# Performance work log

Hardware: AMD Instinct MI355X
Metric: run time of the kernel (lower is better)

Reference implementation:

```python
import jax, jax.numpy as jnp
import numpy as np

N_NODES = 100000
N_EDGES = 1600000
D_IN = 128
D_OUT = 128


def setup_inputs() -> dict:
    key = jax.random.key(0)
    ks = jax.random.split(key, 8)
    h = jax.random.normal(ks[0], (N_NODES, D_IN), dtype=jnp.float32)
    edge_val = jax.random.uniform(ks[1], (N_EDGES,), dtype=jnp.float32)
    # Linear weights in torch layout [out, in]
    W_self = jax.random.normal(ks[2], (D_OUT, D_IN), dtype=jnp.float32) * (1.0 / np.sqrt(D_IN))
    b_self = jax.random.normal(ks[3], (D_OUT,), dtype=jnp.float32) * 0.01
    W_nb = jax.random.normal(ks[4], (D_OUT, D_IN), dtype=jnp.float32) * (1.0 / np.sqrt(D_IN))
    b_nb = jax.random.normal(ks[5], (D_OUT,), dtype=jnp.float32) * 0.01
    edge_row = jax.random.randint(ks[6], (N_EDGES,), 0, N_NODES, dtype=jnp.int64)
    edge_col = jax.random.randint(ks[7], (N_EDGES,), 0, N_NODES, dtype=jnp.int64)
    return {"h": h, "edge_val": edge_val, "W_self": W_self, "b_self": b_self,
            "W_nb": W_nb, "b_nb": b_nb, "edge_row": edge_row, "edge_col": edge_col}


def reference(h, edge_val, W_self, b_self, W_nb, b_nb, edge_row, edge_col):
    # self_h = Linear_self(h[:out_nodes]); out_nodes == N_NODES here
    self_h = h @ W_self.T + b_self  # [N, D_OUT]
    # neighbor_h = adj.spmm(h): sparse COO (row, col, val) times dense h
    msgs = edge_val[:, None] * h[edge_col]            # [E, D_IN]
    neighbor_h = jax.ops.segment_sum(msgs, edge_row, num_segments=N_NODES)  # [N, D_IN]
    out = self_h + neighbor_h @ W_nb.T + b_nb
    return out
```

## Files before the change

kernel.cpp:

```cpp
#include <hip/hip_runtime.h>


constexpr int NN = 100000;
constexpr int NE = 1600000;
constexpr int D  = 128;
constexpr int NBUCK  = 391;
constexpr int BCAP   = 4608;
constexpr int CHUNK  = 4096;
constexpr int NCH    = (NE + CHUNK - 1) / CHUNK;
constexpr int GM     = 64;
constexpr int NGB    = (NN + GM - 1) / GM;
constexpr int LP     = 132;

typedef __bf16 bf16x8 __attribute__((ext_vector_type(8)));
typedef float  f32x4  __attribute__((ext_vector_type(4)));
typedef float  f32x2  __attribute__((ext_vector_type(2)));

__global__ __launch_bounds__(256) void gemm_mfma(
    const float* __restrict__ h,
    const float* __restrict__ Wself,
    const float* __restrict__ Wnb,
    const float* __restrict__ bself,
    const float* __restrict__ bnb,
    float* __restrict__ out,
    __bf16* __restrict__ tmpb)
{
    __shared__ __bf16 hs[GM * LP];
    const int t    = threadIdx.x;
    const int w    = t >> 6;
    const int lane = t & 63;
    const int l15  = lane & 15;
    const int quad = lane >> 4;
    const int row0 = blockIdx.x * GM;

    #pragma unroll
    for (int it = 0; it < 4; ++it) {
        int idx = it * 2048 + t * 8;
        int r = idx >> 7, c = idx & 127;
        int gr = row0 + r; if (gr >= NN) gr = NN - 1;
        f32x4 lo = *(const f32x4*)(h + (size_t)gr * D + c);
        f32x4 hi = *(const f32x4*)(h + (size_t)gr * D + c + 4);
        bf16x8 v;
        #pragma unroll
        for (int j = 0; j < 4; ++j) { v[j] = (__bf16)lo[j]; v[4 + j] = (__bf16)hi[j]; }
        *(bf16x8*)(hs + r * LP + c) = v;
    }

    bf16x8 b[4][4];
    #pragma unroll
    for (int ns = 0; ns < 4; ++ns) {
        int wrow = w * 64 + ns * 16 + l15;
        const float* wr = (wrow < D) ? (Wself + (size_t)wrow * D)
                                     : (Wnb + (size_t)(wrow - D) * D);
        #pragma unroll
        for (int kk = 0; kk < 4; ++kk) {
            f32x4 lo = *(const f32x4*)(wr + kk * 32 + quad * 8);
            f32x4 hi = *(const f32x4*)(wr + kk * 32 + quad * 8 + 4);
            bf16x8 bb;
            #pragma unroll
            for (int j = 0; j < 4; ++j) { bb[j] = (__bf16)lo[j]; bb[4 + j] = (__bf16)hi[j]; }
            b[ns][kk] = bb;
        }
    }
    float bias[4];
    #pragma unroll
    for (int ns = 0; ns < 4; ++ns) {
        int col = w * 64 + ns * 16 + l15;
        bias[ns] = (col < D) ? (bself[col] + bnb[col]) : 0.f;
    }
    __syncthreads();

    f32x4 acc[4][4];
    #pragma unroll
    for (int mi = 0; mi < 4; ++mi)
        #pragma unroll
        for (int ns = 0; ns < 4; ++ns) acc[mi][ns] = (f32x4){0.f, 0.f, 0.f, 0.f};

    #pragma unroll
    for (int mi = 0; mi < 4; ++mi) {
        bf16x8 afr[4];
        #pragma unroll
        for (int kk = 0; kk < 4; ++kk)
            afr[kk] = *(const bf16x8*)(hs + (mi * 16 + l15) * LP + quad * 8 + kk * 32);
        #pragma unroll
        for (int ns = 0; ns < 4; ++ns)
            #pragma unroll
            for (int kk = 0; kk < 4; ++kk)
                acc[mi][ns] = __builtin_amdgcn_mfma_f32_16x16x32_bf16(afr[kk], b[ns][kk], acc[mi][ns], 0, 0, 0);
    }

    #pragma unroll
    for (int mi = 0; mi < 4; ++mi) {
        if (w < 2) {
            #pragma unroll
            for (int ns = 0; ns < 4; ++ns) {
                int col = w * 64 + ns * 16 + l15;
                #pragma unroll
                for (int i = 0; i < 4; ++i) {
                    int row = row0 + mi * 16 + quad * 4 + i;
                    if (row < NN) out[(size_t)row * D + col] = acc[mi][ns][i] + bias[ns];
                }
            }
        } else {
            #pragma unroll
            for (int ns = 0; ns < 4; ++ns) {
                int col = w * 64 + ns * 16 + l15 - D;
                #pragma unroll
                for (int i = 0; i < 4; ++i) {
                    int row = row0 + mi * 16 + quad * 4 + i;
                    if (row < NN) tmpb[(size_t)row * D + col] = (__bf16)acc[mi][ns][i];
                }
            }
        }
    }
}

__global__ __launch_bounds__(512) void wc_scatter(
    const int* __restrict__ erow, const int* __restrict__ ecol,
    const float* __restrict__ eval_,
    int* __restrict__ gcount, int2* __restrict__ epair)
{
    __shared__ int  cnt[NBUCK];
    __shared__ int  lscan[NBUCK];
    __shared__ int  gbase[NBUCK];
    __shared__ int  ss[512];
    __shared__ int2 sbuf[CHUNK];
    __shared__ int  saddr[CHUNK];
    __shared__ int  s_total;

    const int t  = threadIdx.x;
    const int c0 = blockIdx.x * CHUNK;

    for (int b = t; b < NBUCK; b += 512) cnt[b] = 0;
    __syncthreads();

    int   bp[8];
    int   colr[8];
    float valr[8];
    #pragma unroll
    for (int j = 0; j < 8; ++j) {
        int e = c0 + j * 512 + t;
        if (e < NE) {
            int r   = erow[e];
            colr[j] = ecol[e];
            valr[j] = eval_[e];
            int b   = r >> 8;
            int pos = atomicAdd(&cnt[b], 1);
            bp[j]   = b | ((r & 255) << 9) | (pos << 17);
        } else bp[j] = -1;
    }
    __syncthreads();

    ss[t] = (t < NBUCK) ? cnt[t] : 0;
    __syncthreads();
    for (int off = 1; off < 512; off <<= 1) {
        int y = (t >= off) ? ss[t - off] : 0;
        __syncthreads();
        ss[t] += y;
        __syncthreads();
    }
    if (t < NBUCK) {
        int n = cnt[t];
        lscan[t] = ss[t] - n;
        gbase[t] = (n > 0) ? atomicAdd(&gcount[t], n) : 0;
    }
    if (t == 0) s_total = ss[511];
    __syncthreads();

    #pragma unroll
    for (int j = 0; j < 8; ++j) {
        if (bp[j] >= 0) {
            int b   = bp[j] & 511;
            int rlo = (bp[j] >> 9) & 255;
            int pos = bp[j] >> 17;
            int slot = lscan[b] + pos;
            sbuf[slot]  = make_int2(colr[j] | (rlo << 17), __float_as_int(valr[j]));
            saddr[slot] = b * BCAP + gbase[b] + pos;
        }
    }
    __syncthreads();

    int ce = s_total;
    for (int i = t; i < ce; i += 512)
        epair[saddr[i]] = sbuf[i];
}

__global__ __launch_bounds__(512) void bucket_sort(
    const int2* __restrict__ epair, const int* __restrict__ gcount,
    int2* __restrict__ epair2, int2* __restrict__ rowrange)
{
    __shared__ int  cnt[256];
    __shared__ int  off2[256];
    __shared__ int  cur[256];
    __shared__ int  ss[256];
    __shared__ int2 sorted[BCAP];

    const int t = threadIdx.x;
    const int b = blockIdx.x;
    const int n = gcount[b];
    const int2* src = epair + (size_t)b * BCAP;

    if (t < 256) cnt[t] = 0;
    __syncthreads();

    int2 r[9];
    int  nr = 0;
    for (int i = t; i < n; i += 512) {
        int2 p = src[i];
        r[nr++] = p;
        atomicAdd(&cnt[(p.x >> 17) & 255], 1);
    }
    __syncthreads();

    if (t < 256) ss[t] = cnt[t];
    __syncthreads();
    for (int o = 1; o < 256; o <<= 1) {
        int y = 0;
        if (t < 256 && t >= o) y = ss[t - o];
        __syncthreads();
        if (t < 256) ss[t] += y;
        __syncthreads();
    }
    if (t < 256) {
        int v = cnt[t];
        off2[t] = ss[t] - v;
        cur[t]  = ss[t] - v;
    }
    __syncthreads();

    for (int j = 0; j < nr; ++j) {
        int slot = atomicAdd(&cur[(r[j].x >> 17) & 255], 1);
        sorted[slot] = r[j];
    }
    __syncthreads();

    const int base = b * BCAP;
    for (int i = t; i < n; i += 512)
        epair2[base + i] = sorted[i];
    if (t < 256) {
        int row = b * 256 + t;
        if (row < NN)
            rowrange[row] = make_int2(base + off2[t], base + off2[t] + cnt[t]);
    }
}

__global__ __launch_bounds__(256) void aggregate(
    const __bf16* __restrict__ tmpb, const int2* __restrict__ rowrange,
    const int2* __restrict__ epair2, float* __restrict__ out,
    int row0, int nrows)
{
    int wave = row0 + ((blockIdx.x * 256 + threadIdx.x) >> 6);
    if (wave >= row0 + nrows) return;
    int lane = threadIdx.x & 63;
    int2 rr = rowrange[wave];
    int beg = __builtin_amdgcn_readfirstlane(rr.x);
    int end = __builtin_amdgcn_readfirstlane(rr.y);

    float ax[4] = {0.f, 0.f, 0.f, 0.f};
    float ay[4] = {0.f, 0.f, 0.f, 0.f};
    int e = beg;
    for (; e + 3 < end; e += 4) {
        int2 p[4];
        #pragma unroll
        for (int k = 0; k < 4; ++k) p[k] = epair2[e + k];
        #pragma unroll
        for (int k = 0; k < 4; ++k) {
            int col = p[k].x & 0x1FFFF;
            unsigned u = *(const unsigned*)(tmpb + (size_t)col * D + lane * 2);
            float v = __int_as_float(p[k].y);
            ax[k] += v * __uint_as_float(u << 16);
            ay[k] += v * __uint_as_float(u & 0xffff0000u);
        }
    }
    for (; e < end; ++e) {
        int2 p = epair2[e];
        int col = p.x & 0x1FFFF;
        unsigned u = *(const unsigned*)(tmpb + (size_t)col * D + lane * 2);
        float v = __int_as_float(p.y);
        ax[0] += v * __uint_as_float(u << 16);
        ay[0] += v * __uint_as_float(u & 0xffff0000u);
    }
    f32x2* o = (f32x2*)(out + (size_t)wave * D + lane * 2);
    f32x2 c = __builtin_nontemporal_load(o);
    c.x += (ax[0] + ax[1]) + (ax[2] + ax[3]);
    c.y += (ay[0] + ay[1]) + (ay[2] + ay[3]);
    __builtin_nontemporal_store(c, o);
}

extern "C" void kernel_launch(void* const* d_in, const int* in_sizes, int n_in,
                              void* d_out, int out_size, void* d_ws, size_t ws_size,
                              hipStream_t stream) {
    const float* h     = (const float*)d_in[0];
    const float* eval_ = (const float*)d_in[1];
    const float* Wself = (const float*)d_in[2];
    const float* bself = (const float*)d_in[3];
    const float* Wnb   = (const float*)d_in[4];
    const float* bnb   = (const float*)d_in[5];
    const int*   erow  = (const int*)d_in[6];
    const int*   ecol  = (const int*)d_in[7];
    float* out = (float*)d_out;

    char* p = (char*)d_ws;
    __bf16* tmpb    = (__bf16*)p;   p += (size_t)NGB * GM * D * 2;
    int2*   epair   = (int2*)p;     p += (size_t)NBUCK * BCAP * 8;
    int2*   epair2  = (int2*)p;     p += (size_t)NBUCK * BCAP * 8;
    int2*   rowrange= (int2*)p;     p += (size_t)NN * 8;
    int*    gcount  = (int*)p;

    hipMemsetAsync(gcount, 0, NBUCK * 4, stream);

    gemm_mfma<<<NGB, 256, 0, stream>>>(h, Wself, Wnb, bself, bnb, out, tmpb);
    wc_scatter<<<NCH, 512, 0, stream>>>(erow, ecol, eval_, gcount, epair);
    bucket_sort<<<NBUCK, 512, 0, stream>>>(epair, gcount, epair2, rowrange);
    aggregate<<<(50000 * 64) / 256, 256, 0, stream>>>(tmpb, rowrange, epair2, out, 0, 50000);
    aggregate<<<(50000 * 64) / 256, 256, 0, stream>>>(tmpb, rowrange, epair2, out, 50000, 50000);
}
```

Baseline: 265.0 us.

## Double-buffer GEMM tiles, swap MFMA operands for vector stores, rebucket edges into 200-row bins

```diff
diff --git a/kernel.cpp b/kernel.cpp
--- a/kernel.cpp
+++ b/kernel.cpp
@@ -4,17 +4,20 @@
 constexpr int NN = 100000;
 constexpr int NE = 1600000;
 constexpr int D  = 128;
-constexpr int NBUCK  = 391;
-constexpr int BCAP   = 4608;
-constexpr int CHUNK  = 4096;
+constexpr int NBUCK  = 500;
+constexpr int BROWS  = 200;
+constexpr int BCAP   = 3584;
+constexpr int CHUNK  = 2048;
 constexpr int NCH    = (NE + CHUNK - 1) / CHUNK;
 constexpr int GM     = 64;
-constexpr int NGB    = (NN + GM - 1) / GM;
+constexpr int TPB    = 2;
+constexpr int NGB    = (NN + GM * TPB - 1) / (GM * TPB);
 constexpr int LP     = 132;
 
 typedef __bf16 bf16x8 __attribute__((ext_vector_type(8)));
 typedef float  f32x4  __attribute__((ext_vector_type(4)));
 typedef float  f32x2  __attribute__((ext_vector_type(2)));
+typedef unsigned short u16x4 __attribute__((ext_vector_type(4)));
 
 __global__ __launch_bounds__(256) void gemm_mfma(
     const float* __restrict__ h,
@@ -25,28 +28,15 @@
     float* __restrict__ out,
     __bf16* __restrict__ tmpb)
 {
-    __shared__ __bf16 hs[GM * LP];
+    __shared__ __bf16 hs[2][GM * LP];
     const int t    = threadIdx.x;
     const int w    = t >> 6;
     const int lane = t & 63;
     const int l15  = lane & 15;
     const int quad = lane >> 4;
-    const int row0 = blockIdx.x * GM;
-
-    #pragma unroll
-    for (int it = 0; it < 4; ++it) {
-        int idx = it * 2048 + t * 8;
-        int r = idx >> 7, c = idx & 127;
-        int gr = row0 + r; if (gr >= NN) gr = NN - 1;
-        f32x4 lo = *(const f32x4*)(h + (size_t)gr * D + c);
-        f32x4 hi = *(const f32x4*)(h + (size_t)gr * D + c + 4);
-        bf16x8 v;
-        #pragma unroll
-        for (int j = 0; j < 4; ++j) { v[j] = (__bf16)lo[j]; v[4 + j] = (__bf16)hi[j]; }
-        *(bf16x8*)(hs + r * LP + c) = v;
-    }
-
-    bf16x8 b[4][4];
+    const int base_row = blockIdx.x * GM * TPB;
+
+    bf16x8 wf[4][4];
     #pragma unroll
     for (int ns = 0; ns < 4; ++ns) {
         int wrow = w * 64 + ns * 16 + l15;
@@ -59,63 +49,116 @@
             bf16x8 bb;
             #pragma unroll
             for (int j = 0; j < 4; ++j) { bb[j] = (__bf16)lo[j]; bb[4 + j] = (__bf16)hi[j]; }
-            b[ns][kk] = bb;
-        }
-    }
-    float bias[4];
+            wf[ns][kk] = bb;
+        }
+    }
+    f32x4 biasv[4];
     #pragma unroll
     for (int ns = 0; ns < 4; ++ns) {
-        int col = w * 64 + ns * 16 + l15;
-        bias[ns] = (col < D) ? (bself[col] + bnb[col]) : 0.f;
-    }
-    __syncthreads();
-
-    f32x4 acc[4][4];
-    #pragma unroll
-    for (int mi = 0; mi < 4; ++mi)
-        #pragma unroll
-        for (int ns = 0; ns < 4; ++ns) acc[mi][ns] = (f32x4){0.f, 0.f, 0.f, 0.f};
-
-    #pragma unroll
-    for (int mi = 0; mi < 4; ++mi) {
-        bf16x8 afr[4];
-        #pragma unroll
-        for (int kk = 0; kk < 4; ++kk)
-            afr[kk] = *(const bf16x8*)(hs + (mi * 16 + l15) * LP + quad * 8 + kk * 32);
-        #pragma unroll
-        for (int ns = 0; ns < 4; ++ns)
+        int col = w * 64 + ns * 16 + quad * 4;
+        if (col < D) {
+            f32x4 b1 = *(const f32x4*)(bself + col);
+            f32x4 b2 = *(const f32x4*)(bnb + col);
+            biasv[ns] = b1 + b2;
+        } else biasv[ns] = (f32x4){0.f, 0.f, 0.f, 0.f};
+    }
+
+    {
+        #pragma unroll
+        for (int it = 0; it < 4; ++it) {
+            int idx = it * 2048 + t * 8;
+            int r = idx >> 7, c = idx & 127;
+            int gr = base_row + r; if (gr >= NN) gr = NN - 1;
+            f32x4 lo = *(const f32x4*)(h + (size_t)gr * D + c);
+            f32x4 hi = *(const f32x4*)(h + (size_t)gr * D + c + 4);
+            bf16x8 v;
+            #pragma unroll
+            for (int j = 0; j < 4; ++j) { v[j] = (__bf16)lo[j]; v[4 + j] = (__bf16)hi[j]; }
+            *(bf16x8*)(&hs[0][r * LP + c]) = v;
+        }
+    }
+    __syncthreads();
+
+    #pragma unroll
+    for (int tt = 0; tt < TPB; ++tt) {
+        const int row0 = base_row + tt * GM;
+
+        f32x4 pf[8];
+        if (tt + 1 < TPB) {
+            #pragma unroll
+            for (int it = 0; it < 4; ++it) {
+                int idx = it * 2048 + t * 8;
+                int r = idx >> 7, c = idx & 127;
+                int gr = base_row + GM + r; if (gr >= NN) gr = NN - 1;
+                pf[it * 2]     = *(const f32x4*)(h + (size_t)gr * D + c);
+                pf[it * 2 + 1] = *(const f32x4*)(h + (size_t)gr * D + c + 4);
+            }
+        }
+
+        f32x4 acc[4][4];
+        #pragma unroll
+        for (int mi = 0; mi < 4; ++mi)
+            #pragma unroll
+            for (int ns = 0; ns < 4; ++ns) acc[mi][ns] = (f32x4){0.f, 0.f, 0.f, 0.f};
+
+        #pragma unroll
+        for (int mi = 0; mi < 4; ++mi) {
+            bf16x8 hf[4];
             #pragma unroll
             for (int kk = 0; kk < 4; ++kk)
-                acc[mi][ns] = __builtin_amdgcn_mfma_f32_16x16x32_bf16(afr[kk], b[ns][kk], acc[mi][ns], 0, 0, 0);
-    }
-
-    #pragma unroll
-    for (int mi = 0; mi < 4; ++mi) {
-        if (w < 2) {
-            #pragma unroll
-            for (int ns = 0; ns < 4; ++ns) {
-                int col = w * 64 + ns * 16 + l15;
+                hf[kk] = *(const bf16x8*)(&hs[tt & 1][(mi * 16 + l15) * LP + quad * 8 + kk * 32]);
+            #pragma unroll
+            for (int ns = 0; ns < 4; ++ns)
                 #pragma unroll
-                for (int i = 0; i < 4; ++i) {
-                    int row = row0 + mi * 16 + quad * 4 + i;
-                    if (row < NN) out[(size_t)row * D + col] = acc[mi][ns][i] + bias[ns];
+                for (int kk = 0; kk < 4; ++kk)
+                    acc[mi][ns] = __builtin_amdgcn_mfma_f32_16x16x32_bf16(wf[ns][kk], hf[kk], acc[mi][ns], 0, 0, 0);
+        }
+
+        if (tt + 1 < TPB) {
+            #pragma unroll
+            for (int it = 0; it < 4; ++it) {
+                int idx = it * 2048 + t * 8;
+                int r = idx >> 7, c = idx & 127;
+                bf16x8 v;
+                #pragma unroll
+                for (int j = 0; j < 4; ++j) {
+                    v[j]     = (__bf16)pf[it * 2][j];
+                    v[4 + j] = (__bf16)pf[it * 2 + 1][j];
+                }
+                *(bf16x8*)(&hs[(tt + 1) & 1][r * LP + c]) = v;
+            }
+            __syncthreads();
+        }
+
+        #pragma unroll
+        for (int mi = 0; mi < 4; ++mi) {
+            int row = row0 + mi * 16 + l15;
+            if (row < NN) {
+                if (w < 2) {
+                    #pragma unroll
+                    for (int ns = 0; ns < 4; ++ns) {
+                        int col = w * 64 + ns * 16 + quad * 4;
+                        *(f32x4*)(out + (size_t)row * D + col) = acc[mi][ns] + biasv[ns];
+                    }
+                } else {
+                    #pragma unroll
+                    for (int ns = 0; ns < 4; ++ns) {
+                        int col = (w - 2) * 64 + ns * 16 + quad * 4;
+                        u16x4 v;
+                        #pragma unroll
+                        for (int i = 0; i < 4; ++i) {
+                            __bf16 b = (__bf16)acc[mi][ns][i];
+                            v[i] = *(unsigned short*)&b;
+                        }
+                        *(u16x4*)(tmpb + (size_t)row * D + col) = v;
+                    }
                 }
             }
-        } else {
-            #pragma unroll
-            for (int ns = 0; ns < 4; ++ns) {
-                int col = w * 64 + ns * 16 + l15 - D;
-                #pragma unroll
-                for (int i = 0; i < 4; ++i) {
-                    int row = row0 + mi * 16 + quad * 4 + i;
-                    if (row < NN) tmpb[(size_t)row * D + col] = (__bf16)acc[mi][ns][i];
-                }
-            }
-        }
-    }
-}
-
-__global__ __launch_bounds__(512) void wc_scatter(
+        }
+    }
+}
+
+__global__ __launch_bounds__(256) void wc_scatter(
     const int* __restrict__ erow, const int* __restrict__ ecol,
     const float* __restrict__ eval_,
     int* __restrict__ gcount, int2* __restrict__ epair)
@@ -131,7 +174,7 @@
     const int t  = threadIdx.x;
     const int c0 = blockIdx.x * CHUNK;
 
-    for (int b = t; b < NBUCK; b += 512) cnt[b] = 0;
+    for (int b = t; b < NBUCK; b += 256) cnt[b] = 0;
     __syncthreads();
 
     int   bp[8];
@@ -139,30 +182,39 @@
     float valr[8];
     #pragma unroll
     for (int j = 0; j < 8; ++j) {
-        int e = c0 + j * 512 + t;
+        int e = c0 + j * 256 + t;
         if (e < NE) {
             int r   = erow[e];
             colr[j] = ecol[e];
             valr[j] = eval_[e];
-            int b   = r >> 8;
+            int b   = r / BROWS;
+            int rlo = r - b * BROWS;
             int pos = atomicAdd(&cnt[b], 1);
-            bp[j]   = b | ((r & 255) << 9) | (pos << 17);
+            bp[j]   = b | (rlo << 9) | (pos << 17);
         } else bp[j] = -1;
     }
     __syncthreads();
 
-    ss[t] = (t < NBUCK) ? cnt[t] : 0;
+    ss[t]       = (t < NBUCK)       ? cnt[t]       : 0;
+    ss[t + 256] = (t + 256 < NBUCK) ? cnt[t + 256] : 0;
     __syncthreads();
     for (int off = 1; off < 512; off <<= 1) {
-        int y = (t >= off) ? ss[t - off] : 0;
+        int i0 = t, i1 = t + 256;
+        int r0 = ss[i0] + ((i0 >= off) ? ss[i0 - off] : 0);
+        int r1 = ss[i1] + ((i1 >= off) ? ss[i1 - off] : 0);
         __syncthreads();
-        ss[t] += y;
+        ss[i0] = r0; ss[i1] = r1;
         __syncthreads();
     }
     if (t < NBUCK) {
         int n = cnt[t];
         lscan[t] = ss[t] - n;
         gbase[t] = (n > 0) ? atomicAdd(&gcount[t], n) : 0;
+    }
+    if (t + 256 < NBUCK) {
+        int n = cnt[t + 256];
+        lscan[t + 256] = ss[t + 256] - n;
+        gbase[t + 256] = (n > 0) ? atomicAdd(&gcount[t + 256], n) : 0;
     }
     if (t == 0) s_total = ss[511];
     __syncthreads();
@@ -181,7 +233,7 @@
     __syncthreads();
 
     int ce = s_total;
-    for (int i = t; i < ce; i += 512)
+    for (int i = t; i < ce; i += 256)
         epair[saddr[i]] = sbuf[i];
 }
 
@@ -189,9 +241,9 @@
     const int2* __restrict__ epair, const int* __restrict__ gcount,
     int2* __restrict__ epair2, int2* __restrict__ rowrange)
 {
-    __shared__ int  cnt[256];
-    __shared__ int  off2[256];
-    __shared__ int  cur[256];
+    __shared__ int  cnt[BROWS];
+    __shared__ int  off2[BROWS];
+    __shared__ int  cur[BROWS];
     __shared__ int  ss[256];
     __shared__ int2 sorted[BCAP];
 
@@ -200,10 +252,10 @@
     const int n = gcount[b];
     const int2* src = epair + (size_t)b * BCAP;
 
-    if (t < 256) cnt[t] = 0;
-    __syncthreads();
-
-    int2 r[9];
+    if (t < BROWS) cnt[t] = 0;
+    __syncthreads();
+
+    int2 r[8];
     int  nr = 0;
     for (int i = t; i < n; i += 512) {
         int2 p = src[i];
@@ -212,7 +264,7 @@
     }
     __syncthreads();
 
-    if (t < 256) ss[t] = cnt[t];
+    if (t < 256) ss[t] = (t < BROWS) ? cnt[t] : 0;
     __syncthreads();
     for (int o = 1; o < 256; o <<= 1) {
         int y = 0;
@@ -221,7 +273,7 @@
         if (t < 256) ss[t] += y;
         __syncthreads();
     }
-    if (t < 256) {
+    if (t < BROWS) {
         int v = cnt[t];
         off2[t] = ss[t] - v;
         cur[t]  = ss[t] - v;
@@ -237,8 +289,8 @@
     const int base = b * BCAP;
     for (int i = t; i < n; i += 512)
         epair2[base + i] = sorted[i];
-    if (t < 256) {
-        int row = b * 256 + t;
+    if (t < BROWS) {
+        int row = b * BROWS + t;
         if (row < NN)
             rowrange[row] = make_int2(base + off2[t], base + off2[t] + cnt[t]);
     }
@@ -301,7 +353,7 @@
     float* out = (float*)d_out;
 
     char* p = (char*)d_ws;
-    __bf16* tmpb    = (__bf16*)p;   p += (size_t)NGB * GM * D * 2;
+    __bf16* tmpb    = (__bf16*)p;   p += (size_t)(NGB * GM * TPB) * D * 2;
     int2*   epair   = (int2*)p;     p += (size_t)NBUCK * BCAP * 8;
     int2*   epair2  = (int2*)p;     p += (size_t)NBUCK * BCAP * 8;
     int2*   rowrange= (int2*)p;     p += (size_t)NN * 8;
@@ -310,7 +362,7 @@
     hipMemsetAsync(gcount, 0, NBUCK * 4, stream);
 
     gemm_mfma<<<NGB, 256, 0, stream>>>(h, Wself, Wnb, bself, bnb, out, tmpb);
-    wc_scatter<<<NCH, 512, 0, stream>>>(erow, ecol, eval_, gcount, epair);
+    wc_scatter<<<NCH, 256, 0, stream>>>(erow, ecol, eval_, gcount, epair);
     bucket_sort<<<NBUCK, 512, 0, stream>>>(epair, gcount, epair2, rowrange);
     aggregate<<<(50000 * 64) / 256, 256, 0, stream>>>(tmpb, rowrange, epair2, out, 0, 50000);
     aggregate<<<(50000 * 64) / 256, 256, 0, stream>>>(tmpb, rowrange, epair2, out, 50000, 50000);
```

Measured after the change: 263.1 us. About the same (-0.7%).
